# Kernel optimization log

Hardware: AMD Instinct MI355X
Metric: run time of the kernel (lower is better)

## Reference

```python
import jax, jax.numpy as jnp
import numpy as np


def setup_inputs() -> dict:
    key = jax.random.key(0)
    k1, k2, k3, k4 = jax.random.split(key, 4)
    D = 16
    X = jax.random.normal(k1, (512, D), dtype=jnp.float32)
    X2 = jax.random.normal(k2, (512, D), dtype=jnp.float32)
    uls = jax.random.normal(k3, (D,), dtype=jnp.float32)   # unconstrained lengthscales
    uvar = jax.random.normal(k4, (1,), dtype=jnp.float32)  # unconstrained variance
    return {"X": X, "X2": X2, "uls": uls, "uvar": uvar}


def _kernels(X, X2, uls, uvar):
    # softplus-constrained hyperparameters (matches torch softplus/invsoftplus)
    ls = jax.nn.softplus(uls)           # (D,)
    var = jax.nn.softplus(uvar)[0]      # scalar
    N, D = X.shape
    M = X2.shape[0]

    # --- K(X, X2): note original K uses exp(-0.5 * sq_dist / 2) = exp(-0.25*sq) ---
    Xs = X / ls
    X2s = X2 / ls
    sq = (jnp.sum(Xs * Xs, axis=1)[:, None]
          - 2.0 * Xs @ X2s.T
          + jnp.sum(X2s * X2s, axis=1)[None, :])          # (N, M)
    K = var * jnp.exp(-0.25 * sq)                          # (N, M)

    # --- grad_K: analytic d k(x,y)/dx_d = -k * (x_d-y_d)/(2 l_d^2) ---
    # Original: vmap over X2 (outer) and X (inner), grad w.r.t. point in X,
    # then permute(2,1,0).reshape(N*D, M) -> row index = d*N + n.
    diff = (X[:, None, :] - X2[None, :, :]) / (ls * ls)    # (N, M, D)
    gK = -0.5 * diff * K[:, :, None]                       # (N, M, D)
    grad_K = jnp.transpose(gK, (2, 0, 1)).reshape(N * D, M)

    # --- hess_K (X only, use_J=False -> J = I): hess_single = -H where
    # H_ab = d^2 k/dx_a dx_b = k*( (x_a-y_a)(x_b-y_b)/(4 l_a^2 l_b^2) - delta_ab/(2 l_a^2) )
    sqX = (jnp.sum(Xs * Xs, axis=1)[:, None]
           - 2.0 * Xs @ Xs.T
           + jnp.sum(Xs * Xs, axis=1)[None, :])            # (N, N)
    kNN = var * jnp.exp(-0.25 * sqX)                       # (N, N)
    s = (X[:, None, :] - X[None, :, :]) / (ls * ls)        # (N, N, D)
    diag = jnp.diag(0.5 / (ls * ls))                       # (D, D)
    # -H = k * ( delta/(2 l^2) - outer/4 )
    negH = kNN[:, :, None, None] * (diag[None, None, :, :]
                                    - 0.25 * s[:, :, :, None] * s[:, :, None, :])  # (N,N,D,D)
    # original permute(2,0,3,1): index [a*N+i, b*N+j] = -H(X[i], X[j])[a,b]
    hess_K = jnp.transpose(negH, (2, 0, 3, 1)).reshape(N * D, N * D)

    return K, grad_K, hess_K


def reference(X, X2, uls, uvar):
    return _kernels(X, X2, uls, uvar)
```

## Files before the change

### kernel.cpp

```cpp
#include <hip/hip_runtime.h>


#define NN 512
#define DD 16
#define NDD 8192
#define GOFF (NN * NN)
#define HOFF (NN * NN + NDD * NN)

typedef float fv4 __attribute__((ext_vector_type(4)));

__device__ __forceinline__ float softplus_f(float x) {
    return fmaxf(x, 0.0f) + log1pf(expf(-fabsf(x)));
}

__device__ __forceinline__ void store4(float* p, float a, float b, float c, float d) {
    fv4 v = {a, b, c, d};
    *(fv4*)p = v;
}

__device__ __forceinline__ void compute_sk(const float* __restrict__ Xi,
                                           const float* __restrict__ Y0,
                                           const float* __restrict__ s_il2,
                                           float var,
                                           float (&s)[4][DD], float (&k)[4])
{
    float xi[DD];
    const fv4* Xi4 = (const fv4*)Xi;
    #pragma unroll
    for (int c = 0; c < 4; ++c) {
        fv4 v = Xi4[c];
        xi[c * 4 + 0] = v.x; xi[c * 4 + 1] = v.y;
        xi[c * 4 + 2] = v.z; xi[c * 4 + 3] = v.w;
    }
    #pragma unroll
    for (int r = 0; r < 4; ++r) {
        const fv4* Y4 = (const fv4*)(Y0 + r * DD);
        float sq = 0.f;
        #pragma unroll
        for (int c = 0; c < 4; ++c) {
            fv4 v = Y4[c];
            float dif;
            dif = xi[c*4+0] - v.x; s[r][c*4+0] = dif * s_il2[c*4+0]; sq += s[r][c*4+0] * dif;
            dif = xi[c*4+1] - v.y; s[r][c*4+1] = dif * s_il2[c*4+1]; sq += s[r][c*4+1] * dif;
            dif = xi[c*4+2] - v.z; s[r][c*4+2] = dif * s_il2[c*4+2]; sq += s[r][c*4+2] * dif;
            dif = xi[c*4+3] - v.w; s[r][c*4+3] = dif * s_il2[c*4+3]; sq += s[r][c*4+3] * dif;
        }
        k[r] = var * expf(-0.25f * sq);
    }
}

template<int A0>
__device__ __forceinline__ void hess_store(const float (&s)[4][DD], const float (&k)[4],
                                           const float* __restrict__ s_h2,
                                           float* __restrict__ base)
{
    #pragma unroll
    for (int aa = 0; aa < 8; ++aa) {
        const int a = A0 + aa;
        float h2a = s_h2[a];
        float ta0 = -0.25f * k[0] * s[0][a];
        float ta1 = -0.25f * k[1] * s[1][a];
        float ta2 = -0.25f * k[2] * s[2][a];
        float ta3 = -0.25f * k[3] * s[3][a];
        float* row = base + (size_t)a * ((size_t)NN * NDD);
        #pragma unroll
        for (int b = 0; b < DD; ++b) {
            float v0 = ta0 * s[0][b];
            float v1 = ta1 * s[1][b];
            float v2 = ta2 * s[2][b];
            float v3 = ta3 * s[3][b];
            if (b == a) {
                v0 = fmaf(k[0], h2a, v0); v1 = fmaf(k[1], h2a, v1);
                v2 = fmaf(k[2], h2a, v2); v3 = fmaf(k[3], h2a, v3);
            }
            store4(row + (size_t)b * NN, v0, v1, v2, v3);
        }
    }
}

__global__ __launch_bounds__(256) void drbf_kernel(
    const float* __restrict__ X, const float* __restrict__ X2,
    const float* __restrict__ uls, const float* __restrict__ uvar,
    float* __restrict__ out)
{
    __shared__ float s_il2[DD];
    __shared__ float s_h2[DD];
    __shared__ float s_var;
    const int t = threadIdx.x;
    if (t < DD) {
        float ls = softplus_f(uls[t]);
        float il2 = 1.0f / (ls * ls);
        s_il2[t] = il2;
        s_h2[t] = 0.5f * il2;
    }
    if (t == DD) s_var = softplus_f(uvar[0]);
    __syncthreads();
    const float var = s_var;
    const int bx = blockIdx.x;

    if (bx < 512) {
        const int ah = bx >> 8;
        const int h  = (bx & 255) * 256 + t;
        const int j  = (h & 127) * 4;
        const int i  = h >> 7;

        float s[4][DD], k[4];
        compute_sk(X + i * DD, X + j * DD, s_il2, var, s, k);

        float* base = out + HOFF + (size_t)i * NDD + j;
        if (ah == 0) hess_store<0>(s, k, s_h2, base);
        else         hess_store<8>(s, k, s_h2, base);
    } else {
        const int g = (bx - 512) * 256 + t;
        const int m = (g & 127) * 4;
        const int n = g >> 7;

        float s[4][DD], k[4];
        compute_sk(X + n * DD, X2 + m * DD, s_il2, var, s, k);

        store4(out + (size_t)n * NN + m, k[0], k[1], k[2], k[3]);

        #pragma unroll
        for (int d = 0; d < DD; ++d) {
            store4(out + GOFF + (size_t)(d * NN + n) * NN + m,
                   -0.5f * s[0][d] * k[0], -0.5f * s[1][d] * k[1],
                   -0.5f * s[2][d] * k[2], -0.5f * s[3][d] * k[3]);
        }
    }
}

extern "C" void kernel_launch(void* const* d_in, const int* in_sizes, int n_in,
                              void* d_out, int out_size, void* d_ws, size_t ws_size,
                              hipStream_t stream) {
    const float* X    = (const float*)d_in[0];
    const float* X2   = (const float*)d_in[1];
    const float* uls  = (const float*)d_in[2];
    const float* uvar = (const float*)d_in[3];
    float* out = (float*)d_out;
    drbf_kernel<<<dim3(768), dim3(256), 0, stream>>>(X, X2, uls, uvar, out);
}
```

Before: 293.3 us.

## Restructure Hessian output as contiguous row blocks staged through shared memory

```diff
diff --git a/kernel.cpp b/kernel.cpp
--- a/kernel.cpp
+++ b/kernel.cpp
@@ -8,77 +8,22 @@
 #define HOFF (NN * NN + NDD * NN)
 
 typedef float fv4 __attribute__((ext_vector_type(4)));
+typedef float fv2 __attribute__((ext_vector_type(2)));
 
 __device__ __forceinline__ float softplus_f(float x) {
     return fmaxf(x, 0.0f) + log1pf(expf(-fabsf(x)));
 }
 
-__device__ __forceinline__ void store4(float* p, float a, float b, float c, float d) {
-    fv4 v = {a, b, c, d};
-    *(fv4*)p = v;
-}
-
-__device__ __forceinline__ void compute_sk(const float* __restrict__ Xi,
-                                           const float* __restrict__ Y0,
-                                           const float* __restrict__ s_il2,
-                                           float var,
-                                           float (&s)[4][DD], float (&k)[4])
-{
-    float xi[DD];
-    const fv4* Xi4 = (const fv4*)Xi;
+__device__ __forceinline__ void load_row16(const float* __restrict__ p, float (&r)[DD]) {
+    const fv4* p4 = (const fv4*)p;
     #pragma unroll
     for (int c = 0; c < 4; ++c) {
-        fv4 v = Xi4[c];
-        xi[c * 4 + 0] = v.x; xi[c * 4 + 1] = v.y;
-        xi[c * 4 + 2] = v.z; xi[c * 4 + 3] = v.w;
-    }
-    #pragma unroll
-    for (int r = 0; r < 4; ++r) {
-        const fv4* Y4 = (const fv4*)(Y0 + r * DD);
-        float sq = 0.f;
-        #pragma unroll
-        for (int c = 0; c < 4; ++c) {
-            fv4 v = Y4[c];
-            float dif;
-            dif = xi[c*4+0] - v.x; s[r][c*4+0] = dif * s_il2[c*4+0]; sq += s[r][c*4+0] * dif;
-            dif = xi[c*4+1] - v.y; s[r][c*4+1] = dif * s_il2[c*4+1]; sq += s[r][c*4+1] * dif;
-            dif = xi[c*4+2] - v.z; s[r][c*4+2] = dif * s_il2[c*4+2]; sq += s[r][c*4+2] * dif;
-            dif = xi[c*4+3] - v.w; s[r][c*4+3] = dif * s_il2[c*4+3]; sq += s[r][c*4+3] * dif;
-        }
-        k[r] = var * expf(-0.25f * sq);
+        fv4 v = p4[c];
+        r[c*4+0] = v.x; r[c*4+1] = v.y; r[c*4+2] = v.z; r[c*4+3] = v.w;
     }
 }
 
-template<int A0>
-__device__ __forceinline__ void hess_store(const float (&s)[4][DD], const float (&k)[4],
-                                           const float* __restrict__ s_h2,
-                                           float* __restrict__ base)
-{
-    #pragma unroll
-    for (int aa = 0; aa < 8; ++aa) {
-        const int a = A0 + aa;
-        float h2a = s_h2[a];
-        float ta0 = -0.25f * k[0] * s[0][a];
-        float ta1 = -0.25f * k[1] * s[1][a];
-        float ta2 = -0.25f * k[2] * s[2][a];
-        float ta3 = -0.25f * k[3] * s[3][a];
-        float* row = base + (size_t)a * ((size_t)NN * NDD);
-        #pragma unroll
-        for (int b = 0; b < DD; ++b) {
-            float v0 = ta0 * s[0][b];
-            float v1 = ta1 * s[1][b];
-            float v2 = ta2 * s[2][b];
-            float v3 = ta3 * s[3][b];
-            if (b == a) {
-                v0 = fmaf(k[0], h2a, v0); v1 = fmaf(k[1], h2a, v1);
-                v2 = fmaf(k[2], h2a, v2); v3 = fmaf(k[3], h2a, v3);
-            }
-            store4(row + (size_t)b * NN, v0, v1, v2, v3);
-        }
-    }
-}
-
-__global__ __launch_bounds__(256) void drbf_kernel(
+__global__ __launch_bounds__(256, 4) void drbf_kernel(
     const float* __restrict__ X, const float* __restrict__ X2,
     const float* __restrict__ uls, const float* __restrict__ uvar,
     float* __restrict__ out)
@@ -86,45 +31,106 @@
     __shared__ float s_il2[DD];
     __shared__ float s_h2[DD];
     __shared__ float s_var;
+    __shared__ float sS[DD][NN];
+    __shared__ float ta[NN];
+    __shared__ float kk[NN];
+
     const int t = threadIdx.x;
     if (t < DD) {
         float ls = softplus_f(uls[t]);
-        float il2 = 1.0f / (ls * ls);
-        s_il2[t] = il2;
-        s_h2[t] = 0.5f * il2;
+        float i2 = 1.0f / (ls * ls);
+        s_il2[t] = i2;
+        s_h2[t]  = 0.5f * i2;
     }
     if (t == DD) s_var = softplus_f(uvar[0]);
     __syncthreads();
     const float var = s_var;
     const int bx = blockIdx.x;
 
-    if (bx < 512) {
-        const int ah = bx >> 8;
-        const int h  = (bx & 255) * 256 + t;
-        const int j  = (h & 127) * 4;
-        const int i  = h >> 7;
+    if (bx < 8192) {
+        const int a = bx >> 9;
+        const int i = bx & 511;
+        const float h2a = s_h2[a];
 
-        float s[4][DD], k[4];
-        compute_sk(X + i * DD, X + j * DD, s_il2, var, s, k);
+        float xj0[DD], xj1[DD], xi[DD];
+        load_row16(X + (2*t)     * DD, xj0);
+        load_row16(X + (2*t + 1) * DD, xj1);
+        load_row16(X + i * DD, xi);
 
-        float* base = out + HOFF + (size_t)i * NDD + j;
-        if (ah == 0) hess_store<0>(s, k, s_h2, base);
-        else         hess_store<8>(s, k, s_h2, base);
-    } else {
-        const int g = (bx - 512) * 256 + t;
-        const int m = (g & 127) * 4;
-        const int n = g >> 7;
-
-        float s[4][DD], k[4];
-        compute_sk(X + n * DD, X2 + m * DD, s_il2, var, s, k);
-
-        store4(out + (size_t)n * NN + m, k[0], k[1], k[2], k[3]);
-
+        float sq0 = 0.f, sq1 = 0.f, sa0 = 0.f, sa1 = 0.f;
         #pragma unroll
         for (int d = 0; d < DD; ++d) {
-            store4(out + GOFF + (size_t)(d * NN + n) * NN + m,
-                   -0.5f * s[0][d] * k[0], -0.5f * s[1][d] * k[1],
-                   -0.5f * s[2][d] * k[2], -0.5f * s[3][d] * k[3]);
+            float il2 = s_il2[d];
+            float d0 = xi[d] - xj0[d]; float s0 = d0 * il2; sq0 += s0 * d0;
+            float d1 = xi[d] - xj1[d]; float s1 = d1 * il2; sq1 += s1 * d1;
+            if (d == a) { sa0 = s0; sa1 = s1; }
+            ((fv2*)&sS[d][0])[t] = (fv2){s0, s1};
+        }
+        float k0 = var * expf(-0.25f * sq0);
+        float k1 = var * expf(-0.25f * sq1);
+        ((fv2*)ta)[t] = (fv2){-0.25f * k0 * sa0, -0.25f * k1 * sa1};
+        ((fv2*)kk)[t] = (fv2){k0, k1};
+        __syncthreads();
+
+        fv4* row = (fv4*)(out + HOFF + (size_t)bx * NDD);
+        #pragma unroll
+        for (int r = 0; r < 8; ++r) {
+            int c4 = r * 256 + t;
+            int b  = c4 >> 7;
+            int j4 = c4 & 127;
+            fv4 sB = ((const fv4*)&sS[b][0])[j4];
+            fv4 tv = ((const fv4*)ta)[j4];
+            fv4 kv = ((const fv4*)kk)[j4];
+            float dm = (b == a) ? h2a : 0.0f;
+            row[c4] = tv * sB + kv * dm;
+        }
+    } else if (bx < 8192 + 512) {
+        const int beta = bx - 8192;
+        const int dblk = beta >> 5;
+        const int n0   = (beta & 31) * 16;
+
+        float x2a[DD], x2b[DD];
+        load_row16(X2 + t * DD, x2a);
+        load_row16(X2 + (t + 256) * DD, x2b);
+
+        for (int n = n0; n < n0 + 16; ++n) {
+            float xn[DD];
+            load_row16(X + n * DD, xn);
+            float sqa = 0.f, sqb = 0.f, sda = 0.f, sdb = 0.f;
+            #pragma unroll
+            for (int d = 0; d < DD; ++d) {
+                float il2 = s_il2[d];
+                float da = xn[d] - x2a[d]; float sa_ = da * il2; sqa += sa_ * da;
+                float db = xn[d] - x2b[d]; float sb_ = db * il2; sqb += sb_ * db;
+                if (d == dblk) { sda = sa_; sdb = sb_; }
+            }
+            float ka = var * expf(-0.25f * sqa);
+            float kb = var * expf(-0.25f * sqb);
+            float* rowp = out + GOFF + (size_t)(dblk * NN + n) * NN;
+            rowp[t]       = -0.5f * sda * ka;
+            rowp[t + 256] = -0.5f * sdb * kb;
+        }
+    } else {
+        const int beta = bx - 8192 - 512;
+        const int n0 = beta * 16;
+
+        float x2a[DD], x2b[DD];
+        load_row16(X2 + t * DD, x2a);
+        load_row16(X2 + (t + 256) * DD, x2b);
+
+        for (int n = n0; n < n0 + 16; ++n) {
+            float xn[DD];
+            load_row16(X + n * DD, xn);
+            float sqa = 0.f, sqb = 0.f;
+            #pragma unroll
+            for (int d = 0; d < DD; ++d) {
+                float il2 = s_il2[d];
+                float da = xn[d] - x2a[d]; sqa += da * da * il2;
+                float db = xn[d] - x2b[d]; sqb += db * db * il2;
+            }
+            float* rowp = out + (size_t)n * NN;
+            rowp[t]       = var * expf(-0.25f * sqa);
+            rowp[t + 256] = var * expf(-0.25f * sqb);
         }
     }
 }
@@ -137,5 +143,5 @@
     const float* uls  = (const float*)d_in[2];
     const float* uvar = (const float*)d_in[3];
     float* out = (float*)d_out;
-    drbf_kernel<<<dim3(768), dim3(256), 0, stream>>>(X, X2, uls, uvar, out);
+    drbf_kernel<<<dim3(8736), dim3(256), 0, stream>>>(X, X2, uls, uvar, out);
 }
```

After: 299.5 us. 2.1% more time.
